# Kernel tuning notes

Measured on AMD Instinct MI355X. Metric: run time of the kernel, lower is better.

## Reference

```python
import jax, jax.numpy as jnp
import numpy as np


def _l2norm(x, axis=1, eps=1e-12):
    n = jnp.sqrt(jnp.sum(x * x, axis=axis, keepdims=True))
    return x / jnp.maximum(n, eps)


def _update(query, keys, labels, class_counts, num_classes):
    # Vectorized form of Memory.update + get_update_query (train branch).
    m, d = keys.shape
    q = _l2norm(query, axis=1)                              # [N, d]
    score = q @ keys.T                                      # [N, m]
    s_q = jax.nn.softmax(score, axis=0)                     # softmax over queries
    s_m = jax.nn.softmax(score, axis=1)                     # softmax over memory slots
    gather = jnp.argmax(s_m, axis=1)                        # top-1 slot per query, [N]
    # per-slot scatter-reduce: sum_{i: argmax_i==j} s_q[i,j]/max_i s_q[i,j] * q[i]
    w = s_q / jnp.max(s_q, axis=0, keepdims=True)           # [N, m]
    onehot = (gather[:, None] == jnp.arange(m)[None, :]).astype(q.dtype)
    qu = (w * onehot).T @ q                                 # [m, d]
    part = m // num_classes
    slot_class = jnp.arange(m) // part                      # class id of each slot
    active = (slot_class[:, None] == labels[None, :]).any(axis=1)
    qu = jnp.where(active[:, None], qu, 0.0)                # only slots of present classes
    # count-weighted running-average update; torch loop overwrites
    # updated_keys_final each iteration, so only the LAST unique label
    # (torch.unique is sorted -> max) takes effect. Faithful to that.
    last = jnp.max(labels)
    count = jnp.sum(labels == last).astype(q.dtype)
    in_part = slot_class == last
    temp = jnp.where(in_part, class_counts[last], 1.0)[:, None]   # [m, 1]
    updated = temp * keys + qu
    temp2 = temp + jnp.where(in_part, count, 0.0)[:, None]
    return _l2norm(updated / temp2, axis=1)                 # [m, d]


def _read(embedding, mem, num_classes):
    # Memory.read: per-partition block_compare, score is detached in torch.
    m, d = mem.shape
    pr = m // (num_classes - 1)
    nblk = m // pr
    qr = embedding.reshape(d, -1).T                         # [Nq, d]
    blocks = mem.reshape(nblk, pr, d)

    def blk(b):
        s = jax.lax.stop_gradient(b @ qr.T)                 # [pr, Nq] (detached)
        return s.T @ b                                      # [Nq, d]

    return jax.vmap(blk)(blocks)                            # [nblk, Nq, d]


def setup_inputs():
    key = jax.random.key(0)
    k1, k2, k3, k4, k5 = jax.random.split(key, 5)
    N, d, m, C, Nq, L = 8192, 256, 4608, 9, 16384, 16
    return {
        "query": jax.random.normal(k1, (N, d), jnp.float32),
        "embeddings_src": jax.random.normal(k2, (d, Nq), jnp.float32),
        "embeddings_tgt": jax.random.normal(k3, (d, Nq), jnp.float32),
        "keys": _l2norm(jax.random.normal(k4, (m, d), jnp.float32), axis=1),
        "class_counts": jnp.ones((C,), jnp.float32),
        "labels": jax.random.randint(k5, (L,), 1, C).astype(jnp.int32),
        "num_classes": C,
    }


def reference(query, embeddings_src, embeddings_tgt, keys, class_counts, labels, num_classes):
    mem = _update(query, keys, labels, class_counts, num_classes)
    feat_src = _read(embeddings_src, mem, num_classes)
    feat_tgt = _read(embeddings_tgt, mem, num_classes)
    return jnp.stack([feat_src, feat_tgt])                  # [2, nblk, Nq, d]
```

## Files before the change

### kernel.cpp

```cpp
#include <hip/hip_runtime.h>
#include <math.h>

#define NQRY 8192
#define DIM  256
#define MS   4608
#define NQE  16384
#define NBLK 8
#define PRROWS 576

typedef __attribute__((ext_vector_type(8))) short bf16x8;
typedef __attribute__((ext_vector_type(4))) float f32x4;


__device__ __forceinline__ unsigned ordf(float f) {
  unsigned u = __float_as_uint(f);
  return (u & 0x80000000u) ? ~u : (u | 0x80000000u);
}
__device__ __forceinline__ float unordf(unsigned u) {
  unsigned b = (u & 0x80000000u) ? (u & 0x7FFFFFFFu) : ~u;
  return __uint_as_float(b);
}
__device__ __forceinline__ unsigned short bf16rn(float x) {
  unsigned u = __float_as_uint(x);
  unsigned r = u + 0x7FFFu + ((u >> 16) & 1u);
  return (unsigned short)(r >> 16);
}
__device__ __forceinline__ void splitbf(float x, unsigned short& h, unsigned short& lo) {
  unsigned u = __float_as_uint(x);
  h = (unsigned short)(u >> 16);
  float hf = __uint_as_float(u & 0xFFFF0000u);
  lo = bf16rn(x - hf);
}

__global__ __launch_bounds__(256) void k_zero(float4* __restrict__ p, int n4) {
  int i = blockIdx.x * 256 + threadIdx.x;
  if (i < n4) p[i] = float4{0.f, 0.f, 0.f, 0.f};
}

__global__ __launch_bounds__(256) void k_qnorm(const float* __restrict__ query,
                                               float* __restrict__ q,
                                               unsigned short* __restrict__ qh,
                                               unsigned short* __restrict__ ql) {
  int i = blockIdx.x, t = threadIdx.x;
  size_t idx = (size_t)i * DIM + t;
  float x = query[idx];
  float v = x * x;
  #pragma unroll
  for (int o = 32; o; o >>= 1) v += __shfl_down(v, o);
  __shared__ float s[4];
  if ((t & 63) == 0) s[t >> 6] = v;
  __syncthreads();
  float ss = (s[0] + s[1]) + (s[2] + s[3]);
  float qq = x / fmaxf(sqrtf(ss), 1e-12f);
  q[idx] = qq;
  unsigned short h, lo;
  splitbf(qq, h, lo);
  qh[idx] = h; ql[idx] = lo;
}

__global__ __launch_bounds__(256) void k_ksplit(const float* __restrict__ keys,
                                                unsigned short* __restrict__ kh,
                                                unsigned short* __restrict__ kl) {
  size_t idx = (size_t)blockIdx.x * 256 + threadIdx.x;
  unsigned short h, lo;
  splitbf(keys[idx], h, lo);
  kh[idx] = h; kl[idx] = lo;
}

__global__ __launch_bounds__(256) void k_embt(const float* __restrict__ embS,
                                              const float* __restrict__ embT,
                                              unsigned short* __restrict__ ebT) {
  __shared__ float tile[64][33];
  int z = blockIdx.z;
  const float* emb = z ? embT : embS;
  int n0 = blockIdx.x * 32, k0 = blockIdx.y * 64;
  int t = threadIdx.x;
  int kl = t >> 5, nl = t & 31;
  #pragma unroll
  for (int i = 0; i < 8; i++)
    tile[kl * 8 + i][nl] = emb[(size_t)(k0 + kl * 8 + i) * NQE + n0 + nl];
  __syncthreads();
  int nl2 = t >> 3, kq = (t & 7) * 8;
  bf16x8 hv;
  #pragma unroll
  for (int j = 0; j < 8; j++) hv[j] = (short)bf16rn(tile[kq + j][nl2]);
  *(bf16x8*)(ebT + (size_t)z * NQE * DIM + (size_t)(n0 + nl2) * DIM + k0 + kq) = hv;
}

__global__ void k_scalars(const int* __restrict__ labels,
                          const float* __restrict__ cc,
                          float* __restrict__ sc) {
  int t = threadIdx.x;
  int l = (t < 16) ? labels[t] : (int)0x80000000;
  int mx = l;
  #pragma unroll
  for (int o = 32; o; o >>= 1) mx = max(mx, __shfl_down(mx, o));
  mx = __shfl(mx, 0);
  int cnt = (t < 16 && l == mx) ? 1 : 0;
  #pragma unroll
  for (int o = 32; o; o >>= 1) cnt += __shfl_down(cnt, o);
  unsigned amv = (t < 16) ? (1u << l) : 0u;
  #pragma unroll
  for (int o = 32; o; o >>= 1) amv |= __shfl_down(amv, o);
  if (t == 0) {
    sc[0] = __int_as_float(mx);
    sc[1] = (float)cnt;
    sc[2] = cc[mx];
    sc[3] = __uint_as_float(amv);
  }
}

__global__ __launch_bounds__(256) void k_scoremax(
    const unsigned short* __restrict__ qh, const unsigned short* __restrict__ ql,
    const unsigned short* __restrict__ kh, const unsigned short* __restrict__ kl,
    unsigned long long* __restrict__ rowbest, unsigned* __restrict__ colmax) {
  __shared__ __align__(16) char smem[32768];
  char* sA = smem;
  char* sB = smem + 16384;
  int tid = threadIdx.x;
  int n0 = blockIdx.x * 128, m0 = blockIdx.y * 128;
  int w = tid >> 6, lane = tid & 63;
  int wm = w >> 1, wn = w & 1;
  int lr = lane >> 4, lc = lane & 15;
  int srow = tid >> 3, sc8 = tid & 7;
  f32x4 acc[4][4] = {};
  for (int kk = 0; kk < 8; kk++) {
    __syncthreads();
    #pragma unroll
    for (int t = 0; t < 8; t++) {
      int row = (t & 3) * 32 + srow;
      const unsigned short* hi = (t < 4) ? qh : kh;
      const unsigned short* lo = (t < 4) ? ql : kl;
      int base = (t < 4) ? m0 : n0;
      const unsigned short* src =
          ((sc8 < 4) ? hi : lo) + (size_t)(base + row) * DIM + kk * 32 + (sc8 & 3) * 8;
      char* dst = ((t < 4) ? sA : sB) + row * 128 + ((sc8 ^ (row & 7)) << 4);
      *(bf16x8*)dst = *(const bf16x8*)src;
    }
    __syncthreads();
    bf16x8 ah[4], al[4];
    #pragma unroll
    for (int f = 0; f < 4; f++) {
      int ra = wm * 64 + f * 16 + lc;
      ah[f] = *(const bf16x8*)(sA + ra * 128 + ((lr ^ (ra & 7)) << 4));
      al[f] = *(const bf16x8*)(sA + ra * 128 + (((lr + 4) ^ (ra & 7)) << 4));
    }
    #pragma unroll
    for (int half = 0; half < 2; half++) {
      bf16x8 bh[2], bl[2];
      #pragma unroll
      for (int f2 = 0; f2 < 2; f2++) {
        int rb = wn * 64 + (half * 2 + f2) * 16 + lc;
        bh[f2] = *(const bf16x8*)(sB + rb * 128 + ((lr ^ (rb & 7)) << 4));
        bl[f2] = *(const bf16x8*)(sB + rb * 128 + (((lr + 4) ^ (rb & 7)) << 4));
      }
      #pragma unroll
      for (int fm = 0; fm < 4; fm++)
        #pragma unroll
        for (int f2 = 0; f2 < 2; f2++) {
          int fn = half * 2 + f2;
          acc[fm][fn] = __builtin_amdgcn_mfma_f32_16x16x32_bf16(ah[fm], bh[f2], acc[fm][fn], 0, 0, 0);
          acc[fm][fn] = __builtin_amdgcn_mfma_f32_16x16x32_bf16(ah[fm], bl[f2], acc[fm][fn], 0, 0, 0);
          acc[fm][fn] = __builtin_amdgcn_mfma_f32_16x16x32_bf16(al[fm], bh[f2], acc[fm][fn], 0, 0, 0);
        }
    }
  }
  #pragma unroll
  for (int fm = 0; fm < 4; fm++) {
    #pragma unroll
    for (int rg = 0; rg < 4; rg++) {
      unsigned long long p = 0ull;
      #pragma unroll
      for (int fn = 0; fn < 4; fn++) {
        float v = acc[fm][fn][rg];
        unsigned ng = (unsigned)(n0 + wn * 64 + fn * 16 + lc);
        unsigned long long cand =
            ((unsigned long long)ordf(v) << 32) | (unsigned long long)(0xFFFFFFFFu - ng);
        if (cand > p) p = cand;
      }
      #pragma unroll
      for (int o = 1; o < 16; o <<= 1) {
        unsigned long long t2 = __shfl_xor(p, o);
        if (t2 > p) p = t2;
      }
      if (lc == 0)
        atomicMax(rowbest + (m0 + wm * 64 + fm * 16 + lr * 4 + rg), p);
    }
  }
  #pragma unroll
  for (int fn = 0; fn < 4; fn++) {
    float v = -3.4e38f;
    #pragma unroll
    for (int fm = 0; fm < 4; fm++)
      #pragma unroll
      for (int rg = 0; rg < 4; rg++) v = fmaxf(v, acc[fm][fn][rg]);
    v = fmaxf(v, __shfl_xor(v, 16));
    v = fmaxf(v, __shfl_xor(v, 32));
    if (lr == 0) atomicMax(colmax + (n0 + wn * 64 + fn * 16 + lc), ordf(v));
  }
}

__global__ __launch_bounds__(256) void k_rowscatter(
    const unsigned long long* __restrict__ rowbest, const unsigned* __restrict__ colmax,
    const float* __restrict__ q, float* __restrict__ qu) {
  int i = blockIdx.x, t = threadIdx.x;
  unsigned long long p = rowbest[i];
  int g = (int)(0xFFFFFFFFu - (unsigned)(p & 0xFFFFFFFFull));
  float sv = unordf((unsigned)(p >> 32));
  float w = expf(sv - unordf(colmax[g]));
  atomicAdd(qu + (size_t)g * DIM + t, w * q[(size_t)i * DIM + t]);
}

__global__ __launch_bounds__(256) void k_mem(const float* __restrict__ keys,
                                             const float* __restrict__ qu,
                                             const float* __restrict__ sc,
                                             float* __restrict__ memr) {
  int j = blockIdx.x, t = threadIdx.x;
  int last = __float_as_int(sc[0]);
  float count = sc[1], ccl = sc[2];
  unsigned am = __float_as_uint(sc[3]);
  int cls = j >> 9;
  bool inp = (cls == last);
  float temp = inp ? ccl : 1.0f;
  float quv = ((am >> cls) & 1u) ? qu[(size_t)j * DIM + t] : 0.0f;
  float u = temp * keys[(size_t)j * DIM + t] + quv;
  float temp2 = temp + (inp ? count : 0.0f);
  float v = u / temp2;
  float vv = v * v;
  #pragma unroll
  for (int o = 32; o; o >>= 1) vv += __shfl_down(vv, o);
  __shared__ float s[4];
  if ((t & 63) == 0) s[t >> 6] = vv;
  __syncthreads();
  float ss = (s[0] + s[1]) + (s[2] + s[3]);
  memr[(size_t)j * DIM + t] = v / fmaxf(sqrtf(ss), 1e-12f);
}

__global__ __launch_bounds__(256) void k_gram(const float* __restrict__ memr,
                                              unsigned short* __restrict__ Gb) {
  __shared__ float As[16][64];
  __shared__ float Bs[16][64];
  int b = blockIdx.z;
  int kxc = blockIdx.x * 64;
  int kyr = blockIdx.y * 64;
  const float* Ab = memr + (size_t)b * PRROWS * DIM;
  int tid = threadIdx.x, tx = tid & 15, ty = tid >> 4;
  int lp = tid >> 4;
  int lk = (tid & 15) * 4;
  float acc[4][4] = {};
  for (int p0 = 0; p0 < PRROWS; p0 += 16) {
    float4 av = *(const float4*)(Ab + (size_t)(p0 + lp) * DIM + kyr + lk);
    float4 bv = *(const float4*)(Ab + (size_t)(p0 + lp) * DIM + kxc + lk);
    __syncthreads();
    *(float4*)&As[lp][lk] = av;
    *(float4*)&Bs[lp][lk] = bv;
    __syncthreads();
    #pragma unroll
    for (int p = 0; p < 16; p++) {
      float a[4], c[4];
      *(float4*)&a[0] = *(const float4*)&As[p][ty * 4];
      *(float4*)&c[0] = *(const float4*)&Bs[p][tx * 4];
      #pragma unroll
      for (int r = 0; r < 4; r++)
        #pragma unroll
        for (int s2 = 0; s2 < 4; s2++)
          acc[r][s2] = fmaf(a[r], c[s2], acc[r][s2]);
    }
  }
  #pragma unroll
  for (int r = 0; r < 4; r++)
    #pragma unroll
    for (int s2 = 0; s2 < 4; s2++)
      Gb[(size_t)b * DIM * DIM + (size_t)(kyr + ty * 4 + r) * DIM + kxc + tx * 4 + s2] =
          bf16rn(acc[r][s2]);
}

__global__ __launch_bounds__(256) void k_read_mfma(
    const unsigned short* __restrict__ ebT, const unsigned short* __restrict__ Gb,
    float* __restrict__ out) {
  __shared__ __align__(16) char smem[32768];
  char* sA = smem;
  char* sB = smem + 16384;
  int tid = threadIdx.x;
  int eb = blockIdx.z;
  const unsigned short* ea = ebT + (size_t)(eb >> 3) * NQE * DIM;
  const unsigned short* gb = Gb + (size_t)(eb & 7) * DIM * DIM;
  int n0 = blockIdx.x * 128, d0 = blockIdx.y * 128;
  int w = tid >> 6, l = tid & 63;
  int wm = w >> 1, wn = w & 1;
  int lr = l >> 4, lc = l & 15;
  f32x4 acc[4][4] = {};
  for (int kk = 0; kk < 4; kk++) {
    __syncthreads();
    #pragma unroll
    for (int t = 0; t < 4; t++) {
      int c = t * 256 + tid;
      int row = c >> 3, cc = c & 7;
      int ldsb = row * 128 + ((cc * 16) ^ ((row & 7) << 4));
      size_t gA = (size_t)(n0 + row) * DIM + kk * 64 + cc * 8;
      size_t gB = (size_t)(d0 + row) * DIM + kk * 64 + cc * 8;
      *(bf16x8*)(sA + ldsb) = *(const bf16x8*)(ea + gA);
      *(bf16x8*)(sB + ldsb) = *(const bf16x8*)(gb + gB);
    }
    __syncthreads();
    #pragma unroll
    for (int st = 0; st < 2; st++) {
      bf16x8 af[4], bf[4];
      #pragma unroll
      for (int f = 0; f < 4; f++) {
        int ra = wm * 64 + f * 16 + lc;
        int ka = (st * 64 + lr * 16) ^ ((ra & 7) << 4);
        af[f] = *(const bf16x8*)(sA + ra * 128 + ka);
        int rb = wn * 64 + f * 16 + lc;
        int kb = (st * 64 + lr * 16) ^ ((rb & 7) << 4);
        bf[f] = *(const bf16x8*)(sB + rb * 128 + kb);
      }
      #pragma unroll
      for (int fm = 0; fm < 4; fm++)
        #pragma unroll
        for (int fn = 0; fn < 4; fn++)
          acc[fm][fn] = __builtin_amdgcn_mfma_f32_16x16x32_bf16(af[fm], bf[fn], acc[fm][fn], 0, 0, 0);
    }
  }
  size_t base = (size_t)eb * NQE * DIM;
  #pragma unroll
  for (int fm = 0; fm < 4; fm++)
    #pragma unroll
    for (int rg = 0; rg < 4; rg++) {
      int n = n0 + wm * 64 + fm * 16 + lr * 4 + rg;
      float* op = out + base + (size_t)n * DIM + d0 + wn * 64 + lc;
      #pragma unroll
      for (int fn = 0; fn < 4; fn++) op[fn * 16] = acc[fm][fn][rg];
    }
}

extern "C" void kernel_launch(void* const* d_in, const int* in_sizes, int n_in,
                              void* d_out, int out_size, void* d_ws, size_t ws_size,
                              hipStream_t stream) {
  const float* query  = (const float*)d_in[0];
  const float* embS   = (const float*)d_in[1];
  const float* embT   = (const float*)d_in[2];
  const float* keys   = (const float*)d_in[3];
  const float* cc     = (const float*)d_in[4];
  const int*   labels = (const int*)d_in[5];
  float* out = (float*)d_out;

  float* q                     = out;
  unsigned short* qh           = (unsigned short*)(out + 2097152);
  unsigned short* ql           = (unsigned short*)(out + 3145728);
  unsigned short* kh           = (unsigned short*)(out + 4194304);
  unsigned short* kl           = (unsigned short*)(out + 4784128);
  float* qu                    = out + 5373952;
  unsigned long long* rowbest  = (unsigned long long*)(out + 6553600);
  unsigned* colmax             = (unsigned*)(out + 6569984);
  float* memr                  = out + 6574592;

  unsigned short* ebT = (unsigned short*)d_ws;
  unsigned short* Gb  = (unsigned short*)((char*)d_ws + 16777216);
  float* sc           = (float*)((char*)d_ws + 17825792);

  const int n4 = (1179648 + 16384 + 4608) / 4;
  k_zero<<<(n4 + 255) / 256, 256, 0, stream>>>((float4*)qu, n4);

  k_qnorm<<<NQRY, 256, 0, stream>>>(query, q, qh, ql);
  k_ksplit<<<MS, 256, 0, stream>>>(keys, kh, kl);
  k_embt<<<dim3(NQE / 32, DIM / 64, 2), 256, 0, stream>>>(embS, embT, ebT);
  k_scalars<<<1, 64, 0, stream>>>(labels, cc, sc);
  k_scoremax<<<dim3(MS / 128, NQRY / 128), 256, 0, stream>>>(qh, ql, kh, kl, rowbest, colmax);
  k_rowscatter<<<NQRY, 256, 0, stream>>>(rowbest, colmax, q, qu);
  k_mem<<<MS, 256, 0, stream>>>(keys, qu, sc, memr);
  k_gram<<<dim3(4, 4, NBLK), 256, 0, stream>>>(memr, Gb);
  k_read_mfma<<<dim3(NQE / 128, DIM / 128, 2 * NBLK), 256, 0, stream>>>(ebT, Gb, out);
}
```

Measured before the change: 227.3 us.

## Fuse prep kernels into one launch and use 32x32 MFMA for score GEMM

Folds the five preprocessing kernels (zeroing, query normalize/split, key split, embedding transpose, label scalars) into a single block-indexed launch, removing launch gaps and serialization between independent kernels. Separately, the score GEMM switches from 16x16x32 to 32x32x16 bf16 MFMA tiles with reworked fragment loads and epilogue row/column max reductions. The aim is fewer instructions per FLOP and fewer LDS reads. The cost is more complex lane-to-row index mapping and longer reduction shuffles.

```diff
diff --git a/kernel.cpp b/kernel.cpp
--- a/kernel.cpp
+++ b/kernel.cpp
@@ -10,6 +10,7 @@
 
 typedef __attribute__((ext_vector_type(8))) short bf16x8;
 typedef __attribute__((ext_vector_type(4))) float f32x4;
+typedef __attribute__((ext_vector_type(16))) float f32x16;
 
 
 __device__ __forceinline__ unsigned ordf(float f) {
@@ -32,81 +33,78 @@
   lo = bf16rn(x - hf);
 }
 
-__global__ __launch_bounds__(256) void k_zero(float4* __restrict__ p, int n4) {
-  int i = blockIdx.x * 256 + threadIdx.x;
-  if (i < n4) p[i] = float4{0.f, 0.f, 0.f, 0.f};
-}
-
-__global__ __launch_bounds__(256) void k_qnorm(const float* __restrict__ query,
-                                               float* __restrict__ q,
-                                               unsigned short* __restrict__ qh,
-                                               unsigned short* __restrict__ ql) {
-  int i = blockIdx.x, t = threadIdx.x;
-  size_t idx = (size_t)i * DIM + t;
-  float x = query[idx];
-  float v = x * x;
-  #pragma unroll
-  for (int o = 32; o; o >>= 1) v += __shfl_down(v, o);
-  __shared__ float s[4];
-  if ((t & 63) == 0) s[t >> 6] = v;
-  __syncthreads();
-  float ss = (s[0] + s[1]) + (s[2] + s[3]);
-  float qq = x / fmaxf(sqrtf(ss), 1e-12f);
-  q[idx] = qq;
-  unsigned short h, lo;
-  splitbf(qq, h, lo);
-  qh[idx] = h; ql[idx] = lo;
-}
-
-__global__ __launch_bounds__(256) void k_ksplit(const float* __restrict__ keys,
-                                                unsigned short* __restrict__ kh,
-                                                unsigned short* __restrict__ kl) {
-  size_t idx = (size_t)blockIdx.x * 256 + threadIdx.x;
-  unsigned short h, lo;
-  splitbf(keys[idx], h, lo);
-  kh[idx] = h; kl[idx] = lo;
-}
-
-__global__ __launch_bounds__(256) void k_embt(const float* __restrict__ embS,
-                                              const float* __restrict__ embT,
-                                              unsigned short* __restrict__ ebT) {
+#define PREP_NBLK 18070
+#define ZERO_N4   300160
+__global__ __launch_bounds__(256) void k_prep(
+    const float* __restrict__ query, float* __restrict__ q,
+    unsigned short* __restrict__ qh, unsigned short* __restrict__ ql,
+    const float* __restrict__ keys,
+    unsigned short* __restrict__ kh, unsigned short* __restrict__ kl,
+    const float* __restrict__ embS, const float* __restrict__ embT,
+    unsigned short* __restrict__ ebT,
+    float4* __restrict__ zp,
+    const int* __restrict__ labels, const float* __restrict__ cc,
+    float* __restrict__ sc) {
   __shared__ float tile[64][33];
-  int z = blockIdx.z;
-  const float* emb = z ? embT : embS;
-  int n0 = blockIdx.x * 32, k0 = blockIdx.y * 64;
-  int t = threadIdx.x;
-  int kl = t >> 5, nl = t & 31;
-  #pragma unroll
-  for (int i = 0; i < 8; i++)
-    tile[kl * 8 + i][nl] = emb[(size_t)(k0 + kl * 8 + i) * NQE + n0 + nl];
-  __syncthreads();
-  int nl2 = t >> 3, kq = (t & 7) * 8;
-  bf16x8 hv;
-  #pragma unroll
-  for (int j = 0; j < 8; j++) hv[j] = (short)bf16rn(tile[kq + j][nl2]);
-  *(bf16x8*)(ebT + (size_t)z * NQE * DIM + (size_t)(n0 + nl2) * DIM + k0 + kq) = hv;
-}
-
-__global__ void k_scalars(const int* __restrict__ labels,
-                          const float* __restrict__ cc,
-                          float* __restrict__ sc) {
-  int t = threadIdx.x;
-  int l = (t < 16) ? labels[t] : (int)0x80000000;
-  int mx = l;
-  #pragma unroll
-  for (int o = 32; o; o >>= 1) mx = max(mx, __shfl_down(mx, o));
-  mx = __shfl(mx, 0);
-  int cnt = (t < 16 && l == mx) ? 1 : 0;
-  #pragma unroll
-  for (int o = 32; o; o >>= 1) cnt += __shfl_down(cnt, o);
-  unsigned amv = (t < 16) ? (1u << l) : 0u;
-  #pragma unroll
-  for (int o = 32; o; o >>= 1) amv |= __shfl_down(amv, o);
-  if (t == 0) {
-    sc[0] = __int_as_float(mx);
-    sc[1] = (float)cnt;
-    sc[2] = cc[mx];
-    sc[3] = __uint_as_float(amv);
+  int b = blockIdx.x, t = threadIdx.x;
+  if (b < 8192) {
+    size_t idx = (size_t)b * DIM + t;
+    float x = query[idx];
+    float v = x * x;
+    #pragma unroll
+    for (int o = 32; o; o >>= 1) v += __shfl_down(v, o);
+    float* s = &tile[0][0];
+    if ((t & 63) == 0) s[t >> 6] = v;
+    __syncthreads();
+    float ss = (s[0] + s[1]) + (s[2] + s[3]);
+    float qq = x / fmaxf(sqrtf(ss), 1e-12f);
+    q[idx] = qq;
+    unsigned short h, lo;
+    splitbf(qq, h, lo);
+    qh[idx] = h; ql[idx] = lo;
+  } else if (b < 12800) {
+    size_t idx = (size_t)(b - 8192) * 256 + t;
+    unsigned short h, lo;
+    splitbf(keys[idx], h, lo);
+    kh[idx] = h; kl[idx] = lo;
+  } else if (b < 16896) {
+    int bb = b - 12800;
+    int x = bb & 511, y = (bb >> 9) & 3, z = bb >> 11;
+    const float* emb = z ? embT : embS;
+    int n0 = x * 32, k0 = y * 64;
+    int kl2 = t >> 5, nl = t & 31;
+    #pragma unroll
+    for (int i = 0; i < 8; i++)
+      tile[kl2 * 8 + i][nl] = emb[(size_t)(k0 + kl2 * 8 + i) * NQE + n0 + nl];
+    __syncthreads();
+    int nl2 = t >> 3, kq = (t & 7) * 8;
+    bf16x8 hv;
+    #pragma unroll
+    for (int j = 0; j < 8; j++) hv[j] = (short)bf16rn(tile[kq + j][nl2]);
+    *(bf16x8*)(ebT + (size_t)z * NQE * DIM + (size_t)(n0 + nl2) * DIM + k0 + kq) = hv;
+  } else if (b < 18069) {
+    int i = (b - 16896) * 256 + t;
+    if (i < ZERO_N4) zp[i] = float4{0.f, 0.f, 0.f, 0.f};
+  } else {
+    if (t < 64) {
+      int l = (t < 16) ? labels[t] : (int)0x80000000;
+      int mx = l;
+      #pragma unroll
+      for (int o = 32; o; o >>= 1) mx = max(mx, __shfl_down(mx, o));
+      mx = __shfl(mx, 0);
+      int cnt = (t < 16 && l == mx) ? 1 : 0;
+      #pragma unroll
+      for (int o = 32; o; o >>= 1) cnt += __shfl_down(cnt, o);
+      unsigned amv = (t < 16) ? (1u << l) : 0u;
+      #pragma unroll
+      for (int o = 32; o; o >>= 1) amv |= __shfl_down(amv, o);
+      if (t == 0) {
+        sc[0] = __int_as_float(mx);
+        sc[1] = (float)cnt;
+        sc[2] = cc[mx];
+        sc[3] = __uint_as_float(amv);
+      }
+    }
   }
 }
 
@@ -121,82 +119,87 @@
   int n0 = blockIdx.x * 128, m0 = blockIdx.y * 128;
   int w = tid >> 6, lane = tid & 63;
   int wm = w >> 1, wn = w & 1;
-  int lr = lane >> 4, lc = lane & 15;
+  int l31 = lane & 31, hi5 = lane >> 5;
   int srow = tid >> 3, sc8 = tid & 7;
-  f32x4 acc[4][4] = {};
+  f32x16 acc[2][2] = {};
   for (int kk = 0; kk < 8; kk++) {
     __syncthreads();
     #pragma unroll
     for (int t = 0; t < 8; t++) {
       int row = (t & 3) * 32 + srow;
-      const unsigned short* hi = (t < 4) ? qh : kh;
-      const unsigned short* lo = (t < 4) ? ql : kl;
+      const unsigned short* hsrc = (t < 4) ? qh : kh;
+      const unsigned short* lsrc = (t < 4) ? ql : kl;
       int base = (t < 4) ? m0 : n0;
       const unsigned short* src =
-          ((sc8 < 4) ? hi : lo) + (size_t)(base + row) * DIM + kk * 32 + (sc8 & 3) * 8;
+          ((sc8 < 4) ? hsrc : lsrc) + (size_t)(base + row) * DIM + kk * 32 + (sc8 & 3) * 8;
       char* dst = ((t < 4) ? sA : sB) + row * 128 + ((sc8 ^ (row & 7)) << 4);
       *(bf16x8*)dst = *(const bf16x8*)src;
     }
     __syncthreads();
-    bf16x8 ah[4], al[4];
-    #pragma unroll
-    for (int f = 0; f < 4; f++) {
-      int ra = wm * 64 + f * 16 + lc;
-      ah[f] = *(const bf16x8*)(sA + ra * 128 + ((lr ^ (ra & 7)) << 4));
-      al[f] = *(const bf16x8*)(sA + ra * 128 + (((lr + 4) ^ (ra & 7)) << 4));
-    }
-    #pragma unroll
-    for (int half = 0; half < 2; half++) {
+    bf16x8 ah[2][2], al[2][2];
+    #pragma unroll
+    for (int fm = 0; fm < 2; fm++) {
+      int ra = wm * 64 + fm * 32 + l31;
+      #pragma unroll
+      for (int h = 0; h < 2; h++) {
+        int ch = h * 2 + hi5;
+        ah[fm][h] = *(const bf16x8*)(sA + ra * 128 + ((ch ^ (ra & 7)) << 4));
+        al[fm][h] = *(const bf16x8*)(sA + ra * 128 + (((ch + 4) ^ (ra & 7)) << 4));
+      }
+    }
+    #pragma unroll
+    for (int fn = 0; fn < 2; fn++) {
+      int rb = wn * 64 + fn * 32 + l31;
       bf16x8 bh[2], bl[2];
       #pragma unroll
-      for (int f2 = 0; f2 < 2; f2++) {
-        int rb = wn * 64 + (half * 2 + f2) * 16 + lc;
-        bh[f2] = *(const bf16x8*)(sB + rb * 128 + ((lr ^ (rb & 7)) << 4));
-        bl[f2] = *(const bf16x8*)(sB + rb * 128 + (((lr + 4) ^ (rb & 7)) << 4));
-      }
-      #pragma unroll
-      for (int fm = 0; fm < 4; fm++)
+      for (int h = 0; h < 2; h++) {
+        int ch = h * 2 + hi5;
+        bh[h] = *(const bf16x8*)(sB + rb * 128 + ((ch ^ (rb & 7)) << 4));
+        bl[h] = *(const bf16x8*)(sB + rb * 128 + (((ch + 4) ^ (rb & 7)) << 4));
+      }
+      #pragma unroll
+      for (int fm = 0; fm < 2; fm++)
         #pragma unroll
-        for (int f2 = 0; f2 < 2; f2++) {
-          int fn = half * 2 + f2;
-          acc[fm][fn] = __builtin_amdgcn_mfma_f32_16x16x32_bf16(ah[fm], bh[f2], acc[fm][fn], 0, 0, 0);
-          acc[fm][fn] = __builtin_amdgcn_mfma_f32_16x16x32_bf16(ah[fm], bl[f2], acc[fm][fn], 0, 0, 0);
-          acc[fm][fn] = __builtin_amdgcn_mfma_f32_16x16x32_bf16(al[fm], bh[f2], acc[fm][fn], 0, 0, 0);
+        for (int h = 0; h < 2; h++) {
+          acc[fm][fn] = __builtin_amdgcn_mfma_f32_32x32x16_bf16(ah[fm][h], bh[h], acc[fm][fn], 0, 0, 0);
+          acc[fm][fn] = __builtin_amdgcn_mfma_f32_32x32x16_bf16(ah[fm][h], bl[h], acc[fm][fn], 0, 0, 0);
+          acc[fm][fn] = __builtin_amdgcn_mfma_f32_32x32x16_bf16(al[fm][h], bh[h], acc[fm][fn], 0, 0, 0);
         }
     }
   }
   #pragma unroll
-  for (int fm = 0; fm < 4; fm++) {
-    #pragma unroll
-    for (int rg = 0; rg < 4; rg++) {
+  for (int fm = 0; fm < 2; fm++) {
+    #pragma unroll
+    for (int reg = 0; reg < 16; reg++) {
       unsigned long long p = 0ull;
       #pragma unroll
-      for (int fn = 0; fn < 4; fn++) {
-        float v = acc[fm][fn][rg];
-        unsigned ng = (unsigned)(n0 + wn * 64 + fn * 16 + lc);
+      for (int fn = 0; fn < 2; fn++) {
+        float v = acc[fm][fn][reg];
+        unsigned ng = (unsigned)(n0 + wn * 64 + fn * 32 + l31);
         unsigned long long cand =
             ((unsigned long long)ordf(v) << 32) | (unsigned long long)(0xFFFFFFFFu - ng);
         if (cand > p) p = cand;
       }
       #pragma unroll
-      for (int o = 1; o < 16; o <<= 1) {
+      for (int o = 1; o < 32; o <<= 1) {
         unsigned long long t2 = __shfl_xor(p, o);
         if (t2 > p) p = t2;
       }
-      if (lc == 0)
-        atomicMax(rowbest + (m0 + wm * 64 + fm * 16 + lr * 4 + rg), p);
-    }
-  }
-  #pragma unroll
-  for (int fn = 0; fn < 4; fn++) {
+      if (l31 == 0) {
+        int rl = (reg & 3) + 8 * (reg >> 2) + 4 * hi5;
+        atomicMax(rowbest + (m0 + wm * 64 + fm * 32 + rl), p);
+      }
+    }
+  }
+  #pragma unroll
+  for (int fn = 0; fn < 2; fn++) {
     float v = -3.4e38f;
     #pragma unroll
-    for (int fm = 0; fm < 4; fm++)
-      #pragma unroll
-      for (int rg = 0; rg < 4; rg++) v = fmaxf(v, acc[fm][fn][rg]);
-    v = fmaxf(v, __shfl_xor(v, 16));
+    for (int fm = 0; fm < 2; fm++)
+      #pragma unroll
+      for (int reg = 0; reg < 16; reg++) v = fmaxf(v, acc[fm][fn][reg]);
     v = fmaxf(v, __shfl_xor(v, 32));
-    if (lr == 0) atomicMax(colmax + (n0 + wn * 64 + fn * 16 + lc), ordf(v));
+    if (hi5 == 0) atomicMax(colmax + (n0 + wn * 64 + fn * 32 + l31), ordf(v));
   }
 }
 
@@ -359,13 +362,9 @@
   unsigned short* Gb  = (unsigned short*)((char*)d_ws + 16777216);
   float* sc           = (float*)((char*)d_ws + 17825792);
 
-  const int n4 = (1179648 + 16384 + 4608) / 4;
-  k_zero<<<(n4 + 255) / 256, 256, 0, stream>>>((float4*)qu, n4);
-
-  k_qnorm<<<NQRY, 256, 0, stream>>>(query, q, qh, ql);
-  k_ksplit<<<MS, 256, 0, stream>>>(keys, kh, kl);
-  k_embt<<<dim3(NQE / 32, DIM / 64, 2), 256, 0, stream>>>(embS, embT, ebT);
-  k_scalars<<<1, 64, 0, stream>>>(labels, cc, sc);
+  k_prep<<<PREP_NBLK, 256, 0, stream>>>(query, q, qh, ql, keys, kh, kl,
+                                        embS, embT, ebT, (float4*)qu,
+                                        labels, cc, sc);
   k_scoremax<<<dim3(MS / 128, NQRY / 128), 256, 0, stream>>>(qh, ql, kh, kl, rowbest, colmax);
   k_rowscatter<<<NQRY, 256, 0, stream>>>(rowbest, colmax, q, qu);
   k_mem<<<MS, 256, 0, stream>>>(keys, qu, sc, memr);
```

After: 235.1 us. 3.4% more time.
